# Kernel tuning notes

Measured on AMD Instinct MI355X. Metric: run time of the kernel, lower is better.

## Reference

```python
import jax, jax.numpy as jnp
import numpy as np

B, D, L = 32, 576, 196          # batch, literals per patch, patches
Cc, K = 10, 256                 # classes, clauses per class
M = Cc * K                      # total clauses
MASK_DENSITY = 0.02             # fraction of literals included per clause (sparse so clauses actually fire)


def setup_inputs() -> dict:
    key = jax.random.key(0)
    k1, k2, k3 = jax.random.split(key, 3)
    # literals in {0,1} as float (as produced by the upstream TMCNNClass binarizer)
    literals = jax.random.bernoulli(k1, 0.5, (B, D, L)).astype(jnp.float32)
    # sparse clause selection masks [M, D]
    clause_mask = jax.random.uniform(k2, (M, D)) < MASK_DENSITY
    # per-clause vote weights alpha [M]
    alpha = jax.random.normal(k3, (M,), dtype=jnp.float32)
    return {"literals": literals, "clause_mask": clause_mask, "alpha": alpha}


def reference(literals, clause_mask, alpha):
    # Original: lit_masked = where(mask, lit, 1); clause_map = lit_masked.min(dim=D) == 1.
    # With literals in {0,1} this AND-reduce equals: no selected literal is 0, i.e.
    # sum over selected literals of (1 - lit) == 0. Expressed as a GEMM to avoid
    # materializing the B*M*D*L broadcast intermediate.
    mask_f = clause_mask.astype(literals.dtype)                 # [M, D]
    miss = jnp.einsum('md,bdl->bml', mask_f, 1.0 - literals)    # [B, M, L] count of violated literals
    clause_map = miss < 0.5                                     # exact ==0 test on small nonneg ints
    clause_or = jnp.any(clause_map, axis=-1)                    # [B, M] OR over patches

    # Weighted vote: first K/2 clauses per class are positive, second K/2 negative.
    z = clause_or.astype(literals.dtype).reshape(B, Cc, K)      # [B, Cc, K]
    h = K // 2
    sign = jnp.concatenate([jnp.ones((h,), literals.dtype), -jnp.ones((h,), literals.dtype)])
    logits = jnp.einsum('bck,ck->bc', z, alpha.reshape(Cc, K) * sign)  # [B, Cc]
    return clause_map, clause_or, logits
```

## Files before the change

kernel.cpp:

```cpp
#include <hip/hip_runtime.h>
#include <stdint.h>

#define B  32
#define D  576
#define L  196
#define CC 10
#define K  256
#define M  (CC * K)
#define SLOTS 64
#define NF4 49
#define MT 64

#define PACK_BLOCKS ((B * D + 3) / 4)
#define CSR_BLOCKS  ((M + 3) / 4)

__global__ __launch_bounds__(256) void prologue_k(
    const float* __restrict__ lit, const int* __restrict__ mask,
    uint64_t* __restrict__ litbits, int* __restrict__ cnt,
    uint16_t* __restrict__ list) {
    const int lane = threadIdx.x & 63;
    const int wave = threadIdx.x >> 6;

    if (blockIdx.x < PACK_BLOCKS) {
        const int wid = blockIdx.x * 4 + wave;
        if (wid >= B * D) return;
        const int b = wid % B;
        const int d = wid / B;
        const float* base = lit + ((size_t)b * D + d) * L;

        uint64_t w0 = __ballot(base[lane] > 0.5f);
        uint64_t w1 = __ballot(base[64 + lane] > 0.5f);
        uint64_t w2 = __ballot(base[128 + lane] > 0.5f);
        float tail = (lane < 4) ? base[192 + lane] : 0.0f;
        uint64_t w3 = __ballot(tail > 0.5f);

        uint64_t* out = litbits + ((size_t)d * B + b) * 4;
        if (lane == 0) { out[0] = w0; out[1] = w1; out[2] = w2; out[3] = w3; }
    } else {
        const int m = (blockIdx.x - PACK_BLOCKS) * 4 + wave;
        if (m >= M) return;
        const int* row = mask + (size_t)m * D;
        int base = 0;
#pragma unroll
        for (int r = 0; r < 9; ++r) {
            int d = r * 64 + lane;
            bool sel = (row[d] != 0);
            uint64_t bal = __ballot(sel);
            if (sel) {
                int pos = base + __popcll(bal & ((1ull << lane) - 1ull));
                if (pos < SLOTS) list[(size_t)m * SLOTS + pos] = (uint16_t)d;
            }
            base += __popcll(bal);
        }
        if (lane == 0) cnt[m] = (base < SLOTS) ? base : SLOTS;
    }
}

__global__ __launch_bounds__(128) void clause_eval4_k(
    const uint64_t* __restrict__ litbits, const int* __restrict__ cnt,
    const uint16_t* __restrict__ list, float* __restrict__ cmap,
    float* __restrict__ cor) {
    __shared__ uint64_t res[MT * 4];
    __shared__ uint16_t sh_list[MT * SLOTS];
    __shared__ int      sh_cnt[MT];

    const int t  = threadIdx.x;
    const int m0 = blockIdx.x * MT;
    const int b  = blockIdx.y;

    {
        const uint4* lp = (const uint4*)(list + (size_t)m0 * SLOTS);
        uint4* sp = (uint4*)sh_list;
#pragma unroll
        for (int i = t; i < MT * SLOTS * 2 / 16; i += 128) sp[i] = lp[i];
        if (t < MT) sh_cnt[t] = cnt[m0 + t];
    }
    __syncthreads();

    {
        const int c = t >> 1;
        const int h = t & 1;
        const int n = sh_cnt[c];
        const uint16_t* lst = sh_list + c * SLOTS;
        uint64_t a0 = ~0ull, a1 = ~0ull;
        for (int k = 0; k < n; ++k) {
            int d = (int)lst[k];
            const ulonglong2 v =
                *(const ulonglong2*)(litbits + (((size_t)d * B + b) * 4 + 2 * h));
            a0 &= v.x;
            a1 &= v.y;
        }
        res[c * 4 + 2 * h]     = a0;
        res[c * 4 + 2 * h + 1] = a1;
    }
    __syncthreads();

    {
        float4* outp = (float4*)cmap + ((size_t)b * M + m0) * NF4;
        for (int f = t; f < MT * NF4; f += 128) {
            int c  = f / NF4;
            int q  = f - c * NF4;
            int wd = q >> 4;
            int sh = (q & 15) * 4;
            unsigned nib = (unsigned)((res[c * 4 + wd] >> sh) & 0xFull);
            float4 o;
            o.x = (nib & 1u) ? 1.0f : 0.0f;
            o.y = (nib & 2u) ? 1.0f : 0.0f;
            o.z = (nib & 4u) ? 1.0f : 0.0f;
            o.w = (nib & 8u) ? 1.0f : 0.0f;
            outp[f] = o;
        }
    }

    if (t < MT) {
        uint64_t w = res[t * 4] | res[t * 4 + 1] | res[t * 4 + 2] | res[t * 4 + 3];
        cor[(size_t)b * M + m0 + t] = w ? 1.0f : 0.0f;
    }
}

__global__ __launch_bounds__(256) void logits_k(
    const float* __restrict__ cor, const float* __restrict__ alpha,
    float* __restrict__ logits) {
    const int c = blockIdx.x % CC;
    const int b = blockIdx.x / CC;
    const int k = threadIdx.x;
    const float sgn = (k < (K / 2)) ? 1.0f : -1.0f;
    float v = cor[(size_t)b * M + (size_t)c * K + k] * alpha[(size_t)c * K + k] * sgn;
#pragma unroll
    for (int off = 32; off > 0; off >>= 1) v += __shfl_down(v, off, 64);
    __shared__ float sv[4];
    if ((k & 63) == 0) sv[k >> 6] = v;
    __syncthreads();
    if (k == 0) logits[blockIdx.x] = sv[0] + sv[1] + sv[2] + sv[3];
}

extern "C" void kernel_launch(void* const* d_in, const int* in_sizes, int n_in,
                              void* d_out, int out_size, void* d_ws, size_t ws_size,
                              hipStream_t stream) {
    const float* lit   = (const float*)d_in[0];
    const int*   mask  = (const int*)  d_in[1];
    const float* alpha = (const float*)d_in[2];

    float* out    = (float*)d_out;
    float* cmap   = out;
    float* cor    = out + (size_t)B * M * L;
    float* logits = cor + (size_t)B * M;

    uint64_t* litbits = (uint64_t*)d_ws;
    int*      cnt     = (int*)(litbits + (size_t)D * B * 4);
    uint16_t* list    = (uint16_t*)(cnt + M);

    prologue_k<<<PACK_BLOCKS + CSR_BLOCKS, 256, 0, stream>>>(
        lit, mask, litbits, cnt, list);

    clause_eval4_k<<<dim3(M / MT, B), 128, 0, stream>>>(
        litbits, cnt, list, cmap, cor);

    logits_k<<<B * CC, 256, 0, stream>>>(cor, alpha, logits);
}
```

Baseline: 102.4 us.

## Stage per-batch literal bitsets in LDS and transpose clause lists

Bit-packed literals are now laid out batch-major, and each clause-eval block copies its batch's full 576x4-word bitset (18 KB) into shared memory. The literal AND gathers then hit LDS instead of global memory. Clause index lists are transposed in LDS so that lanes handling different clauses read consecutive addresses. Blocks grow to 256 threads, with one 64-bit word per thread. This adds about 27 KB of LDS per block, which may limit occupancy, and every block reloads the bitset even though the gathers are sparse.

After: 101.5 us. About the same (-0.9%).

```diff
diff --git a/kernel.cpp b/kernel.cpp
--- a/kernel.cpp
+++ b/kernel.cpp
@@ -34,7 +34,7 @@
         float tail = (lane < 4) ? base[192 + lane] : 0.0f;
         uint64_t w3 = __ballot(tail > 0.5f);
 
-        uint64_t* out = litbits + ((size_t)d * B + b) * 4;
+        uint64_t* out = litbits + ((size_t)b * D + d) * 4;
         if (lane == 0) { out[0] = w0; out[1] = w1; out[2] = w2; out[3] = w3; }
     } else {
         const int m = (blockIdx.x - PACK_BLOCKS) * 4 + wave;
@@ -56,12 +56,13 @@
     }
 }
 
-__global__ __launch_bounds__(128) void clause_eval4_k(
+__global__ __launch_bounds__(256) void clause_eval5_k(
     const uint64_t* __restrict__ litbits, const int* __restrict__ cnt,
     const uint16_t* __restrict__ list, float* __restrict__ cmap,
     float* __restrict__ cor) {
+    __shared__ uint64_t lit_s[D * 4];
+    __shared__ uint16_t listT[SLOTS * MT];
     __shared__ uint64_t res[MT * 4];
-    __shared__ uint16_t sh_list[MT * SLOTS];
     __shared__ int      sh_cnt[MT];
 
     const int t  = threadIdx.x;
@@ -69,35 +70,44 @@
     const int b  = blockIdx.y;
 
     {
+        const uint4* gp = (const uint4*)(litbits + (size_t)b * D * 4);
+        uint4* sp = (uint4*)lit_s;
+#pragma unroll
+        for (int i = 0; i < 4; ++i) sp[t + 256 * i] = gp[t + 256 * i];
+        if (t < D * 2 - 1024) sp[1024 + t] = gp[1024 + t];
+    }
+    {
         const uint4* lp = (const uint4*)(list + (size_t)m0 * SLOTS);
-        uint4* sp = (uint4*)sh_list;
 #pragma unroll
-        for (int i = t; i < MT * SLOTS * 2 / 16; i += 128) sp[i] = lp[i];
+        for (int i = 0; i < 2; ++i) {
+            int idx = t + 256 * i;
+            uint4 v = lp[idx];
+            const uint16_t* e = (const uint16_t*)&v;
+            int c  = idx >> 3;
+            int s0 = (idx & 7) * 8;
+#pragma unroll
+            for (int j = 0; j < 8; ++j) listT[(s0 + j) * MT + c] = e[j];
+        }
         if (t < MT) sh_cnt[t] = cnt[m0 + t];
     }
     __syncthreads();
 
     {
-        const int c = t >> 1;
-        const int h = t & 1;
+        const int c = t >> 2;
+        const int h = t & 3;
         const int n = sh_cnt[c];
-        const uint16_t* lst = sh_list + c * SLOTS;
-        uint64_t a0 = ~0ull, a1 = ~0ull;
+        uint64_t a = ~0ull;
         for (int k = 0; k < n; ++k) {
-            int d = (int)lst[k];
-            const ulonglong2 v =
-                *(const ulonglong2*)(litbits + (((size_t)d * B + b) * 4 + 2 * h));
-            a0 &= v.x;
-            a1 &= v.y;
+            int d = (int)listT[k * MT + c];
+            a &= lit_s[d * 4 + h];
         }
-        res[c * 4 + 2 * h]     = a0;
-        res[c * 4 + 2 * h + 1] = a1;
+        res[t] = a;
     }
     __syncthreads();
 
     {
         float4* outp = (float4*)cmap + ((size_t)b * M + m0) * NF4;
-        for (int f = t; f < MT * NF4; f += 128) {
+        for (int f = t; f < MT * NF4; f += 256) {
             int c  = f / NF4;
             int q  = f - c * NF4;
             int wd = q >> 4;
@@ -113,7 +123,8 @@
     }
 
     if (t < MT) {
-        uint64_t w = res[t * 4] | res[t * 4 + 1] | res[t * 4 + 2] | res[t * 4 + 3];
+        uint64_t w = res[t * 4] | res[t * 4 + 1] | res[t * 4 + 2] |
+                     (res[t * 4 + 3] & 0xFull);
         cor[(size_t)b * M + m0 + t] = w ? 1.0f : 0.0f;
     }
 }
@@ -147,13 +158,13 @@
     float* logits = cor + (size_t)B * M;
 
     uint64_t* litbits = (uint64_t*)d_ws;
-    int*      cnt     = (int*)(litbits + (size_t)D * B * 4);
+    int*      cnt     = (int*)(litbits + (size_t)B * D * 4);
     uint16_t* list    = (uint16_t*)(cnt + M);
 
     prologue_k<<<PACK_BLOCKS + CSR_BLOCKS, 256, 0, stream>>>(
         lit, mask, litbits, cnt, list);
 
-    clause_eval4_k<<<dim3(M / MT, B), 128, 0, stream>>>(
+    clause_eval5_k<<<dim3(M / MT, B), 256, 0, stream>>>(
         litbits, cnt, list, cmap, cor);
 
     logits_k<<<B * CC, 256, 0, stream>>>(cor, alpha, logits);
```
